# Performance work log

Hardware: AMD Instinct MI355X
Metric: run time of the kernel (lower is better)

The kernel has to match this reference:

```python
import jax, jax.numpy as jnp
import numpy as np

EPS = 1e-5

def layer_norm(x, gamma, beta):
    mu = jnp.mean(x, axis=-1, keepdims=True)
    var = jnp.mean(jnp.square(x - mu), axis=-1, keepdims=True)
    return (x - mu) * jax.lax.rsqrt(var + EPS) * gamma + beta

def setup_inputs() -> dict:
    key = jax.random.key(0)
    ks = jax.random.split(key, 16)
    B, Cq, Hq, Wq = 8, 256, 32, 32
    Cc, Hc, Wc = 512, 64, 64
    def lin(k, fan_in, fan_out):
        lim = 1.0 / np.sqrt(fan_in)
        k1, k2 = jax.random.split(k)
        W = jax.random.uniform(k1, (fan_in, fan_out), jnp.float32, -lim, lim)
        b = jax.random.uniform(k2, (fan_out,), jnp.float32, -lim, lim)
        return W, b
    Wq_, bq = lin(ks[0], Cq, Cq)
    Wk_, bk = lin(ks[1], Cc, Cq)
    Wv_, bv = lin(ks[2], Cc, Cq)
    Wo_, bo = lin(ks[3], Cq, Cq)
    return {
        "query": jax.random.normal(ks[4], (B, Cq, Hq, Wq), jnp.float32),
        "context": jax.random.normal(ks[5], (B, Cc, Hc, Wc), jnp.float32),
        "Wq": Wq_, "bq": bq, "Wk": Wk_, "bk": bk, "Wv": Wv_, "bv": bv,
        "Wo": Wo_, "bo": bo,
        "gq": jnp.ones((Cq,), jnp.float32), "betq": jnp.zeros((Cq,), jnp.float32),
        "gc": jnp.ones((Cc,), jnp.float32), "betc": jnp.zeros((Cc,), jnp.float32),
    }

def reference(query, context, Wq, bq, Wk, bk, Wv, bv, Wo, bo, gq, betq, gc, betc):
    B, Cq, Hq, Wq_sp = query.shape
    _, Cc, Hc, Wc = context.shape
    num_heads = 8
    head_dim = Cq // num_heads
    scale = jnp.sqrt(jnp.float32(head_dim))
    N = Hq * Wq_sp
    # adaptive_avg_pool2d with divisible sizes == average pooling over equal bins
    ctx = context.reshape(B, Cc, Hq, Hc // Hq, Wq_sp, Wc // Wq_sp).mean(axis=(3, 5))
    q_flat = query.reshape(B, Cq, N).transpose(0, 2, 1)          # (B,N,Cq)
    c_flat = ctx.reshape(B, Cc, N).transpose(0, 2, 1)            # (B,N,Cc)
    qn = layer_norm(q_flat, gq, betq)
    cn = layer_norm(c_flat, gc, betc)
    q = (qn @ Wq + bq).reshape(B, N, num_heads, head_dim).transpose(0, 2, 1, 3)
    k = (cn @ Wk + bk).reshape(B, N, num_heads, head_dim).transpose(0, 2, 1, 3)
    v = (cn @ Wv + bv).reshape(B, N, num_heads, head_dim).transpose(0, 2, 1, 3)
    attn = jnp.einsum('bhnd,bhmd->bhnm', q, k) / scale
    attn = jax.nn.softmax(attn, axis=-1)
    out = jnp.einsum('bhnm,bhmd->bhnd', attn, v)
    out = out.transpose(0, 2, 1, 3).reshape(B, N, Cq)
    out = out @ Wo + bo
    out = q_flat + out                                           # residual
    return out.transpose(0, 2, 1).reshape(B, Cq, Hq, Wq_sp)
```

## Files before the change

### kernel.cpp

```cpp
#include <hip/hip_runtime.h>
#include <hip/hip_bf16.h>
#include <cstddef>

#define B_  8
#define CQ  256
#define CC  512
#define N_  1024
#define HQ  32
#define WQ  32
#define NH  8
#define HD  32

typedef __bf16 bf16x8 __attribute__((ext_vector_type(8)));
typedef float f32x4 __attribute__((ext_vector_type(4)));
typedef float f32x16 __attribute__((ext_vector_type(16)));
typedef unsigned int uint4v __attribute__((ext_vector_type(4)));
typedef unsigned short ushort8 __attribute__((ext_vector_type(8)));
typedef unsigned short ushort4v __attribute__((ext_vector_type(4)));

__device__ __forceinline__ unsigned short f2bf(float x) {
    return __builtin_bit_cast(unsigned short, __float2bfloat16(x));
}
__device__ __forceinline__ float bf2f(unsigned short x) {
    return __bfloat162float(__builtin_bit_cast(__hip_bfloat16, x));
}
__device__ __forceinline__ bf16x8 ldb8(const unsigned short* p) {
    return __builtin_bit_cast(bf16x8, *(const ushort8*)p);
}

__global__ __launch_bounds__(256) void prep_k(
    const float* __restrict__ query, const float* __restrict__ context,
    const float* __restrict__ Wq, const float* __restrict__ Wk,
    const float* __restrict__ Wv, const float* __restrict__ Wo,
    const float* __restrict__ gq, const float* __restrict__ betq,
    const float* __restrict__ gc, const float* __restrict__ betc,
    __hip_bfloat16* __restrict__ Wqt, __hip_bfloat16* __restrict__ Wkt,
    __hip_bfloat16* __restrict__ Wvt, __hip_bfloat16* __restrict__ Wot,
    __hip_bfloat16* __restrict__ qn, __hip_bfloat16* __restrict__ cn) {
    __shared__ float T[32][33];
    __shared__ float SsA[32][16];
    __shared__ float S2A[32][16];
    __shared__ float SsB[16][64];
    __shared__ float S2B[16][64];
    __shared__ float Mu[64], Rs[64];

    const int bid = blockIdx.x;
    const int tid = threadIdx.x;

    if (bid < 512) {
        const int x = bid & 15, y = (bid >> 4) & 7, z = bid >> 7;
        const float* W; __hip_bfloat16* Wt; int K;
        switch (z) {
            case 0: W = Wq; Wt = Wqt; K = CQ; break;
            case 1: W = Wk; Wt = Wkt; K = CC; break;
            case 2: W = Wv; Wt = Wvt; K = CC; break;
            default: W = Wo; Wt = Wot; K = CQ; break;
        }
        const int k0 = x * 32;
        if (k0 >= K) return;
        const int c0 = y * 32;
        const int tx = tid & 31, ty = tid >> 5;
        #pragma unroll
        for (int i = 0; i < 4; ++i) {
            const int r = ty + 8 * i;
            T[r][tx] = W[(size_t)(k0 + r) * CQ + c0 + tx];
        }
        __syncthreads();
        #pragma unroll
        for (int i = 0; i < 4; ++i) {
            const int r = ty + 8 * i;
            Wt[(size_t)(c0 + r) * K + k0 + tx] = __float2bfloat16(T[tx][r]);
        }
    } else if (bid < 1024) {
        const int u    = bid - 512;
        const int wqc2 = u & 1, hq = (u >> 1) & 31, b = u >> 6;
        const int pp   = tid & 7;
        const int cg   = tid >> 3;
        const int ch0  = cg * 16;

        const float* Cb = context + ((size_t)b * CC + ch0) * 4096
                        + (size_t)(2 * hq) * 64 + (32 * wqc2 + 4 * pp);
        float pv0[16], pv1[16];
        float ss0 = 0.f, ss1 = 0.f, s20 = 0.f, s21 = 0.f;
        #pragma unroll
        for (int i = 0; i < 16; ++i) {
            const float4 r0 = *(const float4*)(Cb + (size_t)i * 4096);
            const float4 r1 = *(const float4*)(Cb + (size_t)i * 4096 + 64);
            const float v0 = (r0.x + r0.y + r1.x + r1.y) * 0.25f;
            const float v1 = (r0.z + r0.w + r1.z + r1.w) * 0.25f;
            pv0[i] = v0; pv1[i] = v1;
            ss0 += v0; s20 += v0 * v0;
            ss1 += v1; s21 += v1 * v1;
        }
        SsA[cg][2 * pp]     = ss0; S2A[cg][2 * pp]     = s20;
        SsA[cg][2 * pp + 1] = ss1; S2A[cg][2 * pp + 1] = s21;
        __syncthreads();
        if (tid < 16) {
            float ts = 0.f, t2 = 0.f;
            #pragma unroll
            for (int i = 0; i < 32; ++i) { ts += SsA[i][tid]; t2 += S2A[i][tid]; }
            const float mu  = ts * (1.f / CC);
            const float var = t2 * (1.f / CC) - mu * mu;
            Mu[tid] = mu; Rs[tid] = rsqrtf(var + 1e-5f);
        }
        __syncthreads();
        const float mu0 = Mu[2 * pp],     rs0 = Rs[2 * pp];
        const float mu1 = Mu[2 * pp + 1], rs1 = Rs[2 * pp + 1];
        const int pos0 = hq * 32 + wqc2 * 16 + 2 * pp;
        unsigned short* dst = (unsigned short*)cn
            + ((size_t)b * N_ + pos0) * CC + ch0;
        ushort8 a0, a1, b0, b1;
        #pragma unroll
        for (int i = 0; i < 8; ++i) {
            a0[i] = f2bf((pv0[i] - mu0) * rs0 * gc[ch0 + i] + betc[ch0 + i]);
            b0[i] = f2bf((pv1[i] - mu1) * rs1 * gc[ch0 + i] + betc[ch0 + i]);
        }
        #pragma unroll
        for (int i = 0; i < 8; ++i) {
            a1[i] = f2bf((pv0[8 + i] - mu0) * rs0 * gc[ch0 + 8 + i] + betc[ch0 + 8 + i]);
            b1[i] = f2bf((pv1[8 + i] - mu1) * rs1 * gc[ch0 + 8 + i] + betc[ch0 + 8 + i]);
        }
        *(ushort8*)(dst)          = a0;
        *(ushort8*)(dst + 8)      = a1;
        *(ushort8*)(dst + CC)     = b0;
        *(ushort8*)(dst + CC + 8) = b1;
    } else {
        const int u  = bid - 1024;
        const int nt = u & 15, b = u >> 4;
        const int nq = tid & 15;
        const int cg = tid >> 4;
        const int ch0 = cg * 16;
        const int nb  = nt * 64 + 4 * nq;

        const float* Qb = query + ((size_t)b * CQ + ch0) * N_ + nb;
        float qv[64];
        float ps[4] = {0.f, 0.f, 0.f, 0.f};
        float p2[4] = {0.f, 0.f, 0.f, 0.f};
        #pragma unroll
        for (int i = 0; i < 16; ++i) {
            const float4 v = *(const float4*)(Qb + (size_t)i * N_);
            qv[4 * i + 0] = v.x; qv[4 * i + 1] = v.y;
            qv[4 * i + 2] = v.z; qv[4 * i + 3] = v.w;
            ps[0] += v.x; p2[0] += v.x * v.x;
            ps[1] += v.y; p2[1] += v.y * v.y;
            ps[2] += v.z; p2[2] += v.z * v.z;
            ps[3] += v.w; p2[3] += v.w * v.w;
        }
        #pragma unroll
        for (int j = 0; j < 4; ++j) {
            SsB[cg][4 * nq + j] = ps[j];
            S2B[cg][4 * nq + j] = p2[j];
        }
        __syncthreads();
        if (tid < 64) {
            float ts = 0.f, t2 = 0.f;
            #pragma unroll
            for (int i = 0; i < 16; ++i) { ts += SsB[i][tid]; t2 += S2B[i][tid]; }
            const float mu  = ts * (1.f / CQ);
            const float var = t2 * (1.f / CQ) - mu * mu;
            Mu[tid] = mu; Rs[tid] = rsqrtf(var + 1e-5f);
        }
        __syncthreads();
        #pragma unroll
        for (int j = 0; j < 4; ++j) {
            const float mu = Mu[4 * nq + j], rs = Rs[4 * nq + j];
            ushort8 o0, o1;
            #pragma unroll
            for (int i = 0; i < 8; ++i)
                o0[i] = f2bf((qv[4 * i + j] - mu) * rs * gq[ch0 + i] + betq[ch0 + i]);
            #pragma unroll
            for (int i = 0; i < 8; ++i)
                o1[i] = f2bf((qv[4 * (8 + i) + j] - mu) * rs * gq[ch0 + 8 + i] + betq[ch0 + 8 + i]);
            unsigned short* dst = (unsigned short*)qn
                + ((size_t)b * N_ + nb + j) * CQ + ch0;
            *(ushort8*)(dst)     = o0;
            *(ushort8*)(dst + 8) = o1;
        }
    }
}

__global__ __launch_bounds__(256) void proj_all_k(
    const __hip_bfloat16* __restrict__ qn, const __hip_bfloat16* __restrict__ cn,
    const __hip_bfloat16* __restrict__ Wqt, const __hip_bfloat16* __restrict__ Wkt,
    const __hip_bfloat16* __restrict__ Wvt,
    const float* __restrict__ bq, const float* __restrict__ bk,
    const float* __restrict__ bv,
    __hip_bfloat16* __restrict__ Qb, __hip_bfloat16* __restrict__ Kb,
    __hip_bfloat16* __restrict__ Vt, float qsc) {
    __shared__ unsigned short As[64][40];
    __shared__ unsigned short B1[64][40];
    __shared__ unsigned short B2[64][40];

    const int zz = blockIdx.z;
    const int n0 = blockIdx.x * 64;
    const int c0 = blockIdx.y * 64;
    const int tid = threadIdx.x;
    const int wid = tid >> 6, lane = tid & 63;
    const int lg = lane >> 4, ln = lane & 15;
    const int wn0 = (wid & 1) * 32, wc0 = (wid >> 1) * 32;
    const int sr = tid >> 2;
    const int sk = (tid & 3) * 8;

    if (zz >= 8) {
        const int b = zz - 8;
        const unsigned short* Ab = (const unsigned short*)qn + ((size_t)b * N_ + n0) * CQ;
        const unsigned short* Wb = (const unsigned short*)Wqt + (size_t)c0 * CQ;
        f32x4 acc[2][2] = {};
        ushort8 ra = *(const ushort8*)(Ab + (size_t)sr * CQ + sk);
        ushort8 rw = *(const ushort8*)(Wb + (size_t)sr * CQ + sk);
        for (int t = 0; t < 8; ++t) {
            *(ushort8*)&As[sr][sk] = ra;
            *(ushort8*)&B1[sr][sk] = rw;
            __syncthreads();
            if (t < 7) {
                ra = *(const ushort8*)(Ab + (size_t)sr * CQ + (t + 1) * 32 + sk);
                rw = *(const ushort8*)(Wb + (size_t)sr * CQ + (t + 1) * 32 + sk);
            }
            bf16x8 a[2], w[2];
            #pragma unroll
            for (int i = 0; i < 2; ++i) a[i] = ldb8(&As[wn0 + 16 * i + ln][8 * lg]);
            #pragma unroll
            for (int j = 0; j < 2; ++j) w[j] = ldb8(&B1[wc0 + 16 * j + ln][8 * lg]);
            #pragma unroll
            for (int i = 0; i < 2; ++i)
                #pragma unroll
                for (int j = 0; j < 2; ++j)
                    acc[i][j] = __builtin_amdgcn_mfma_f32_16x16x32_bf16(a[i], w[j], acc[i][j], 0, 0, 0);
            __syncthreads();
        }
        #pragma unroll
        for (int j = 0; j < 2; ++j) {
            const int co = c0 + wc0 + 16 * j + ln;
            const int h = co >> 5, d = co & 31;
            const float bb = bq[co];
            #pragma unroll
            for (int i = 0; i < 2; ++i)
                #pragma unroll
                for (int r = 0; r < 4; ++r) {
                    const int n = n0 + wn0 + 16 * i + 4 * lg + r;
                    Qb[(((size_t)b * NH + h) * N_ + n) * HD + d] =
                        __float2bfloat16((acc[i][j][r] + bb) * qsc);
                }
        }
    } else {
        const int b = zz;
        const unsigned short* Ab  = (const unsigned short*)cn + ((size_t)b * N_ + n0) * CC;
        const unsigned short* Wkb = (const unsigned short*)Wkt + (size_t)c0 * CC;
        const unsigned short* Wvb = (const unsigned short*)Wvt + (size_t)c0 * CC;
        f32x4 accK[2][2] = {};
        f32x4 accV[2][2] = {};
        ushort8 ra = *(const ushort8*)(Ab  + (size_t)sr * CC + sk);
        ushort8 rk = *(const ushort8*)(Wkb + (size_t)sr * CC + sk);
        ushort8 rv = *(const ushort8*)(Wvb + (size_t)sr * CC + sk);
        for (int t = 0; t < 16; ++t) {
            *(ushort8*)&As[sr][sk] = ra;
            *(ushort8*)&B1[sr][sk] = rk;
            *(ushort8*)&B2[sr][sk] = rv;
            __syncthreads();
            if (t < 15) {
                ra = *(const ushort8*)(Ab  + (size_t)sr * CC + (t + 1) * 32 + sk);
                rk = *(const ushort8*)(Wkb + (size_t)sr * CC + (t + 1) * 32 + sk);
                rv = *(const ushort8*)(Wvb + (size_t)sr * CC + (t + 1) * 32 + sk);
            }
            bf16x8 a[2], wk[2], wv[2];
            #pragma unroll
            for (int i = 0; i < 2; ++i) {
                a[i]  = ldb8(&As[wn0 + 16 * i + ln][8 * lg]);
                wk[i] = ldb8(&B1[wc0 + 16 * i + ln][8 * lg]);
                wv[i] = ldb8(&B2[wc0 + 16 * i + ln][8 * lg]);
            }
            #pragma unroll
            for (int i = 0; i < 2; ++i)
                #pragma unroll
                for (int j = 0; j < 2; ++j) {
                    accK[i][j] = __builtin_amdgcn_mfma_f32_16x16x32_bf16(a[i], wk[j], accK[i][j], 0, 0, 0);
                    accV[i][j] = __builtin_amdgcn_mfma_f32_16x16x32_bf16(a[i], wv[j], accV[i][j], 0, 0, 0);
                }
            __syncthreads();
        }
        #pragma unroll
        for (int j = 0; j < 2; ++j) {
            const int co = c0 + wc0 + 16 * j + ln;
            const int h = co >> 5, d = co & 31;
            const float bbk = bk[co], bbv = bv[co];
            #pragma unroll
            for (int i = 0; i < 2; ++i) {
                const int nb = n0 + wn0 + 16 * i + 4 * lg;
                #pragma unroll
                for (int r = 0; r < 4; ++r)
                    Kb[(((size_t)b * NH + h) * N_ + nb + r) * HD + d] =
                        __float2bfloat16(accK[i][j][r] + bbk);
                ushort4v o;
                #pragma unroll
                for (int r = 0; r < 4; ++r) o[r] = f2bf(accV[i][j][r] + bbv);
                const int g  = (nb >> 2) & 3;
                const int gp = ((g & 1) << 1) | (g >> 1);
                const int nbp = (nb & ~15) | (gp << 2);
                *(ushort4v*)((unsigned short*)Vt + (((size_t)b * NH + h) * HD + d) * N_ + nbp) = o;
            }
        }
    }
}

__global__ __launch_bounds__(256) void attn32_k(
    const __hip_bfloat16* __restrict__ Q,
    const __hip_bfloat16* __restrict__ K,
    const __hip_bfloat16* __restrict__ Vt,
    __hip_bfloat16* __restrict__ O) {
    __shared__ float accS[2][64][20];
    __shared__ float lwS[2][64];

    const int lin = blockIdx.x + 16 * blockIdx.y;
    const int eff = (lin & 7) * 128 + (lin >> 3);
    const int qt  = eff & 15;
    const int bh  = eff >> 4;
    const int b   = bh >> 3;
    const int h   = bh & 7;
    const int wid  = threadIdx.x >> 6;
    const int lane = threadIdx.x & 63;
    const int l31  = lane & 31;
    const int hh   = lane >> 5;
    const int qsub = wid >> 1;
    const int kvh  = wid & 1;
    const int q0   = qt * 64 + qsub * 32;

    const unsigned short* Qp = (const unsigned short*)Q + ((size_t)bh * N_ + q0) * HD;
    const unsigned short* Kbb = (const unsigned short*)K + (size_t)bh * N_ * HD;
    const unsigned short* Vb = (const unsigned short*)Vt + ((size_t)bh * HD + l31) * N_;

    bf16x8 qB[2];
    #pragma unroll
    for (int m = 0; m < 2; ++m)
        qB[m] = ldb8(Qp + (size_t)l31 * HD + 16 * m + 8 * hh);

    const f32x16 Z = {0.f,0.f,0.f,0.f,0.f,0.f,0.f,0.f,
                      0.f,0.f,0.f,0.f,0.f,0.f,0.f,0.f};
    f32x16 acc = Z;
    float ls0 = 0.f, ls1 = 0.f, ls2 = 0.f, ls3 = 0.f;

    const int kvbase = kvh * 512;
    const unsigned short* kp = Kbb + (size_t)(kvbase + l31) * HD + 8 * hh;
    const unsigned short* vp = Vb + kvbase + 8 * hh;

    bf16x8 kaA[2][4];
    #pragma unroll
    for (int j = 0; j < 4; ++j)
        kaA[0][j] = ldb8(kp + (j >> 1) * 1024 + (j & 1) * 16);

    #pragma unroll
    for (int st = 0; st < 8; ++st) {
        const int cur = st & 1;
        bf16x8 va[4];
        #pragma unroll
        for (int j = 0; j < 4; ++j)
            va[j] = ldb8(vp + st * 64 + 16 * j);
        if (st < 7) {
            const unsigned short* kp2 = kp + (size_t)(st + 1) * 2048;
            #pragma unroll
            for (int j = 0; j < 4; ++j)
                kaA[cur ^ 1][j] = ldb8(kp2 + (j >> 1) * 1024 + (j & 1) * 16);
        }

        f32x16 s0, s1;
        s0 = __builtin_amdgcn_mfma_f32_32x32x16_bf16(kaA[cur][0], qB[0], Z, 0, 0, 0);
        s0 = __builtin_amdgcn_mfma_f32_32x32x16_bf16(kaA[cur][1], qB[1], s0, 0, 0, 0);
        s1 = __builtin_amdgcn_mfma_f32_32x32x16_bf16(kaA[cur][2], qB[0], Z, 0, 0, 0);
        s1 = __builtin_amdgcn_mfma_f32_32x32x16_bf16(kaA[cur][3], qB[1], s1, 0, 0, 0);

        unsigned int pk[2][4][2];
        #pragma unroll
        for (int T = 0; T < 2; ++T) {
            float p[16];
            #pragma unroll
            for (int r = 0; r < 16; ++r)
                p[r] = __builtin_amdgcn_exp2f(T == 0 ? s0[r] : s1[r]);
            #pragma unroll
            for (int r = 0; r < 16; r += 4) {
                ls0 += p[r]; ls1 += p[r + 1]; ls2 += p[r + 2]; ls3 += p[r + 3];
            }
            #pragma unroll
            for (int c = 0; c < 4; ++c) {
                asm("v_cvt_pk_bf16_f32 %0, %1, %2"
                    : "=v"(pk[T][c][0]) : "v"(p[4 * c]), "v"(p[4 * c + 1]));
                asm("v_cvt_pk_bf16_f32 %0, %1, %2"
                    : "=v"(pk[T][c][1]) : "v"(p[4 * c + 2]), "v"(p[4 * c + 3]));
            }
        }

        #pragma unroll
        for (int w = 0; w < 4; ++w) {
            const int T = w >> 1, cp = w & 1;
            uint4v fu = {pk[T][2 * cp][0], pk[T][2 * cp][1],
                         pk[T][2 * cp + 1][0], pk[T][2 * cp + 1][1]};
            const bf16x8 pa = __builtin_bit_cast(bf16x8, fu);
            acc = __builtin_amdgcn_mfma_f32_32x32x16_bf16(pa, va[w], acc, 0, 0, 0);
        }
    }

    const float lsum = (ls0 + ls1) + (ls2 + ls3);
    const float lw = lsum + __shfl_xor(lsum, 32);

    if (kvh == 1) {
        #pragma unroll
        for (int r4 = 0; r4 < 4; ++r4) {
            float4 v = {acc[4 * r4], acc[4 * r4 + 1], acc[4 * r4 + 2], acc[4 * r4 + 3]};
            *(float4*)&accS[qsub][lane][4 * r4] = v;
        }
        lwS[qsub][lane] = lw;
    }
    __syncthreads();
    if (kvh == 0) {
        const float linv = 1.0f / (lw + lwS[qsub][lane]);
        #pragma unroll
        for (int r = 0; r < 16; ++r) {
            const int ql = (r & 3) + 8 * (r >> 2) + 4 * hh;
            const float vv = (acc[r] + accS[qsub][lane][r]) * __shfl(linv, ql);
            O[((size_t)b * N_ + q0 + ql) * CQ + h * HD + l31] = __float2bfloat16(vv);
        }
    }
}

__global__ __launch_bounds__(256) void out_proj_k(const __hip_bfloat16* __restrict__ Ob,
                              const __hip_bfloat16* __restrict__ Wot,
                              const float* __restrict__ bo,
                              const float* __restrict__ query,
                              float* __restrict__ out) {
    __shared__ unsigned short As[64][40];
    __shared__ unsigned short Bs[64][40];
    const int b  = blockIdx.z;
    const int n0 = blockIdx.x * 64;
    const int c0 = blockIdx.y * 64;
    const int tid = threadIdx.x;
    const int wid = tid >> 6, lane = tid & 63;
    const int lg = lane >> 4, ln = lane & 15;
    const int wn0 = (wid & 1) * 32, wc0 = (wid >> 1) * 32;

    const unsigned short* Ab = (const unsigned short*)Ob + ((size_t)b * N_ + n0) * CQ;
    const unsigned short* Wb = (const unsigned short*)Wot + (size_t)c0 * CQ;
    const int sr = tid >> 2;
    const int sk = (tid & 3) * 8;

    f32x4 acc[2][2] = {};
    ushort8 ra = *(const ushort8*)(Ab + (size_t)sr * CQ + sk);
    ushort8 rw = *(const ushort8*)(Wb + (size_t)sr * CQ + sk);

    for (int t = 0; t < 8; ++t) {
        *(ushort8*)&As[sr][sk] = ra;
        *(ushort8*)&Bs[sr][sk] = rw;
        __syncthreads();
        if (t < 7) {
            ra = *(const ushort8*)(Ab + (size_t)sr * CQ + (t + 1) * 32 + sk);
            rw = *(const ushort8*)(Wb + (size_t)sr * CQ + (t + 1) * 32 + sk);
        }
        bf16x8 a[2], w[2];
        #pragma unroll
        for (int i = 0; i < 2; ++i)
            a[i] = ldb8(&As[wn0 + 16 * i + ln][8 * lg]);
        #pragma unroll
        for (int j = 0; j < 2; ++j)
            w[j] = ldb8(&Bs[wc0 + 16 * j + ln][8 * lg]);
        #pragma unroll
        for (int i = 0; i < 2; ++i)
            #pragma unroll
            for (int j = 0; j < 2; ++j)
                acc[i][j] = __builtin_amdgcn_mfma_f32_16x16x32_bf16(a[i], w[j], acc[i][j], 0, 0, 0);
        __syncthreads();
    }

    #pragma unroll
    for (int j = 0; j < 2; ++j) {
        const int co = c0 + wc0 + 16 * j + ln;
        const float bb = bo[co];
        #pragma unroll
        for (int i = 0; i < 2; ++i) {
            const int nb = n0 + wn0 + 16 * i + 4 * lg;
            const float4 res = *(const float4*)&query[((size_t)b * CQ + co) * N_ + nb];
            float4 o;
            o.x = acc[i][j][0] + bb + res.x;
            o.y = acc[i][j][1] + bb + res.y;
            o.z = acc[i][j][2] + bb + res.z;
            o.w = acc[i][j][3] + bb + res.w;
            *(float4*)&out[((size_t)b * CQ + co) * N_ + nb] = o;
        }
    }
}

extern "C" void kernel_launch(void* const* d_in, const int* in_sizes, int n_in,
                              void* d_out, int out_size, void* d_ws, size_t ws_size,
                              hipStream_t stream) {
    const float* query   = (const float*)d_in[0];
    const float* context = (const float*)d_in[1];
    const float* Wq = (const float*)d_in[2];
    const float* bq = (const float*)d_in[3];
    const float* Wk = (const float*)d_in[4];
    const float* bk = (const float*)d_in[5];
    const float* Wv = (const float*)d_in[6];
    const float* bv = (const float*)d_in[7];
    const float* Wo = (const float*)d_in[8];
    const float* bo = (const float*)d_in[9];
    const float* gq   = (const float*)d_in[10];
    const float* betq = (const float*)d_in[11];
    const float* gc   = (const float*)d_in[12];
    const float* betc = (const float*)d_in[13];
    float* out = (float*)d_out;

    char* w = (char*)d_ws;
    __hip_bfloat16* qn  = (__hip_bfloat16*)w;  w += (size_t)B_ * N_ * CQ * 2;
    __hip_bfloat16* cn  = (__hip_bfloat16*)w;  w += (size_t)B_ * N_ * CC * 2;
    __hip_bfloat16* Qb  = (__hip_bfloat16*)w;  w += (size_t)B_ * NH * N_ * HD * 2;
    __hip_bfloat16* Kb  = (__hip_bfloat16*)w;  w += (size_t)B_ * NH * N_ * HD * 2;
    __hip_bfloat16* Vt  = (__hip_bfloat16*)w;  w += (size_t)B_ * NH * HD * N_ * 2;
    __hip_bfloat16* Ob  = (__hip_bfloat16*)w;  w += (size_t)B_ * N_ * CQ * 2;
    __hip_bfloat16* Wqt = (__hip_bfloat16*)w;  w += (size_t)CQ * CQ * 2;
    __hip_bfloat16* Wkt = (__hip_bfloat16*)w;  w += (size_t)CQ * CC * 2;
    __hip_bfloat16* Wvt = (__hip_bfloat16*)w;  w += (size_t)CQ * CC * 2;
    __hip_bfloat16* Wot = (__hip_bfloat16*)w;  w += (size_t)CQ * CQ * 2;

    prep_k<<<dim3(1152), 256, 0, stream>>>(query, context, Wq, Wk, Wv, Wo,
                                           gq, betq, gc, betc,
                                           Wqt, Wkt, Wvt, Wot, qn, cn);

    const float qsc = 0.17677669529663687f * 1.4426950408889634f;
    proj_all_k<<<dim3(16, 4, 16), 256, 0, stream>>>(qn, cn, Wqt, Wkt, Wvt,
                                                    bq, bk, bv, Qb, Kb, Vt, qsc);

    attn32_k<<<dim3(16, 64), 256, 0, stream>>>(Qb, Kb, Vt, Ob);

    out_proj_k<<<dim3(16, 4, 8), 256, 0, stream>>>(Ob, Wot, bo, query, out);
}
```

Before: 66.68 us.

## Widen projection GEMM tiles to 128 columns and use bf16 residual copy

The Q/K/V and output projection GEMMs now use 64x128 output tiles per block (each wave computes 32x64), halving the grid in the channel dimension and reusing each loaded A tile across twice as many output columns. Separately, prep_k writes a bf16 copy of the raw query, which the output projection reads for the residual instead of the fp32 query, halving residual read bytes. The wider tiles raise register use and cut block count to 512/256, which may lower occupancy. The bf16 residual loses precision in the residual add and adds an extra write in prep.

```diff
diff --git a/kernel.cpp b/kernel.cpp
--- a/kernel.cpp
+++ b/kernel.cpp
@@ -36,7 +36,8 @@
     const float* __restrict__ gc, const float* __restrict__ betc,
     __hip_bfloat16* __restrict__ Wqt, __hip_bfloat16* __restrict__ Wkt,
     __hip_bfloat16* __restrict__ Wvt, __hip_bfloat16* __restrict__ Wot,
-    __hip_bfloat16* __restrict__ qn, __hip_bfloat16* __restrict__ cn) {
+    __hip_bfloat16* __restrict__ qn, __hip_bfloat16* __restrict__ cn,
+    __hip_bfloat16* __restrict__ qraw) {
     __shared__ float T[32][33];
     __shared__ float SsA[32][16];
     __shared__ float S2A[32][16];
@@ -147,6 +148,13 @@
             ps[3] += v.w; p2[3] += v.w * v.w;
         }
         #pragma unroll
+        for (int i = 0; i < 16; ++i) {
+            ushort4v o;
+            o[0] = f2bf(qv[4 * i + 0]); o[1] = f2bf(qv[4 * i + 1]);
+            o[2] = f2bf(qv[4 * i + 2]); o[3] = f2bf(qv[4 * i + 3]);
+            *(ushort4v*)((unsigned short*)qraw + ((size_t)b * CQ + ch0 + i) * N_ + nb) = o;
+        }
+        #pragma unroll
         for (int j = 0; j < 4; ++j) {
             SsB[cg][4 * nq + j] = ps[j];
             S2B[cg][4 * nq + j] = p2[j];
@@ -188,48 +196,54 @@
     __hip_bfloat16* __restrict__ Qb, __hip_bfloat16* __restrict__ Kb,
     __hip_bfloat16* __restrict__ Vt, float qsc) {
     __shared__ unsigned short As[64][40];
-    __shared__ unsigned short B1[64][40];
-    __shared__ unsigned short B2[64][40];
+    __shared__ unsigned short B1[128][40];
+    __shared__ unsigned short B2[128][40];
 
     const int zz = blockIdx.z;
     const int n0 = blockIdx.x * 64;
-    const int c0 = blockIdx.y * 64;
+    const int c0 = blockIdx.y * 128;
     const int tid = threadIdx.x;
     const int wid = tid >> 6, lane = tid & 63;
     const int lg = lane >> 4, ln = lane & 15;
-    const int wn0 = (wid & 1) * 32, wc0 = (wid >> 1) * 32;
+    const int wn0 = (wid & 1) * 32, wc0 = (wid >> 1) * 64;
     const int sr = tid >> 2;
     const int sk = (tid & 3) * 8;
+    const int br = tid >> 1;
+    const int bk0 = (tid & 1) * 16;
 
     if (zz >= 8) {
         const int b = zz - 8;
         const unsigned short* Ab = (const unsigned short*)qn + ((size_t)b * N_ + n0) * CQ;
         const unsigned short* Wb = (const unsigned short*)Wqt + (size_t)c0 * CQ;
-        f32x4 acc[2][2] = {};
-        ushort8 ra = *(const ushort8*)(Ab + (size_t)sr * CQ + sk);
-        ushort8 rw = *(const ushort8*)(Wb + (size_t)sr * CQ + sk);
+        f32x4 acc[2][4] = {};
+        ushort8 ra  = *(const ushort8*)(Ab + (size_t)sr * CQ + sk);
+        ushort8 rw0 = *(const ushort8*)(Wb + (size_t)br * CQ + bk0);
+        ushort8 rw1 = *(const ushort8*)(Wb + (size_t)br * CQ + bk0 + 8);
         for (int t = 0; t < 8; ++t) {
-            *(ushort8*)&As[sr][sk] = ra;
-            *(ushort8*)&B1[sr][sk] = rw;
+            *(ushort8*)&As[sr][sk]      = ra;
+            *(ushort8*)&B1[br][bk0]     = rw0;
+            *(ushort8*)&B1[br][bk0 + 8] = rw1;
             __syncthreads();
             if (t < 7) {
-                ra = *(const ushort8*)(Ab + (size_t)sr * CQ + (t + 1) * 32 + sk);
-                rw = *(const ushort8*)(Wb + (size_t)sr * CQ + (t + 1) * 32 + sk);
+                const int k0 = (t + 1) * 32;
+                ra  = *(const ushort8*)(Ab + (size_t)sr * CQ + k0 + sk);
+                rw0 = *(const ushort8*)(Wb + (size_t)br * CQ + k0 + bk0);
+                rw1 = *(const ushort8*)(Wb + (size_t)br * CQ + k0 + bk0 + 8);
             }
-            bf16x8 a[2], w[2];
+            bf16x8 a[2], w[4];
             #pragma unroll
             for (int i = 0; i < 2; ++i) a[i] = ldb8(&As[wn0 + 16 * i + ln][8 * lg]);
             #pragma unroll
-            for (int j = 0; j < 2; ++j) w[j] = ldb8(&B1[wc0 + 16 * j + ln][8 * lg]);
+            for (int j = 0; j < 4; ++j) w[j] = ldb8(&B1[wc0 + 16 * j + ln][8 * lg]);
             #pragma unroll
             for (int i = 0; i < 2; ++i)
                 #pragma unroll
-                for (int j = 0; j < 2; ++j)
+                for (int j = 0; j < 4; ++j)
                     acc[i][j] = __builtin_amdgcn_mfma_f32_16x16x32_bf16(a[i], w[j], acc[i][j], 0, 0, 0);
             __syncthreads();
         }
         #pragma unroll
-        for (int j = 0; j < 2; ++j) {
+        for (int j = 0; j < 4; ++j) {
             const int co = c0 + wc0 + 16 * j + ln;
             const int h = co >> 5, d = co & 31;
             const float bb = bq[co];
@@ -247,39 +261,47 @@
         const unsigned short* Ab  = (const unsigned short*)cn + ((size_t)b * N_ + n0) * CC;
         const unsigned short* Wkb = (const unsigned short*)Wkt + (size_t)c0 * CC;
         const unsigned short* Wvb = (const unsigned short*)Wvt + (size_t)c0 * CC;
-        f32x4 accK[2][2] = {};
-        f32x4 accV[2][2] = {};
-        ushort8 ra = *(const ushort8*)(Ab  + (size_t)sr * CC + sk);
-        ushort8 rk = *(const ushort8*)(Wkb + (size_t)sr * CC + sk);
-        ushort8 rv = *(const ushort8*)(Wvb + (size_t)sr * CC + sk);
+        f32x4 accK[2][4] = {};
+        f32x4 accV[2][4] = {};
+        ushort8 ra  = *(const ushort8*)(Ab  + (size_t)sr * CC + sk);
+        ushort8 rk0 = *(const ushort8*)(Wkb + (size_t)br * CC + bk0);
+        ushort8 rk1 = *(const ushort8*)(Wkb + (size_t)br * CC + bk0 + 8);
+        ushort8 rv0 = *(const ushort8*)(Wvb + (size_t)br * CC + bk0);
+        ushort8 rv1 = *(const ushort8*)(Wvb + (size_t)br * CC + bk0 + 8);
         for (int t = 0; t < 16; ++t) {
-            *(ushort8*)&As[sr][sk] = ra;
-            *(ushort8*)&B1[sr][sk] = rk;
-            *(ushort8*)&B2[sr][sk] = rv;
+            *(ushort8*)&As[sr][sk]      = ra;
+            *(ushort8*)&B1[br][bk0]     = rk0;
+            *(ushort8*)&B1[br][bk0 + 8] = rk1;
+            *(ushort8*)&B2[br][bk0]     = rv0;
+            *(ushort8*)&B2[br][bk0 + 8] = rv1;
             __syncthreads();
             if (t < 15) {
-                ra = *(const ushort8*)(Ab  + (size_t)sr * CC + (t + 1) * 32 + sk);
-                rk = *(const ushort8*)(Wkb + (size_t)sr * CC + (t + 1) * 32 + sk);
-                rv = *(const ushort8*)(Wvb + (size_t)sr * CC + (t + 1) * 32 + sk);
+                const int k0 = (t + 1) * 32;
+                ra  = *(const ushort8*)(Ab  + (size_t)sr * CC + k0 + sk);
+                rk0 = *(const ushort8*)(Wkb + (size_t)br * CC + k0 + bk0);
+                rk1 = *(const ushort8*)(Wkb + (size_t)br * CC + k0 + bk0 + 8);
+                rv0 = *(const ushort8*)(Wvb + (size_t)br * CC + k0 + bk0);
+                rv1 = *(const ushort8*)(Wvb + (size_t)br * CC + k0 + bk0 + 8);
             }
-            bf16x8 a[2], wk[2], wv[2];
-            #pragma unroll
-            for (int i = 0; i < 2; ++i) {
-                a[i]  = ldb8(&As[wn0 + 16 * i + ln][8 * lg]);
-                wk[i] = ldb8(&B1[wc0 + 16 * i + ln][8 * lg]);
-                wv[i] = ldb8(&B2[wc0 + 16 * i + ln][8 * lg]);
+            bf16x8 a[2], wk[4], wv[4];
+            #pragma unroll
+            for (int i = 0; i < 2; ++i) a[i] = ldb8(&As[wn0 + 16 * i + ln][8 * lg]);
+            #pragma unroll
+            for (int j = 0; j < 4; ++j) {
+                wk[j] = ldb8(&B1[wc0 + 16 * j + ln][8 * lg]);
+                wv[j] = ldb8(&B2[wc0 + 16 * j + ln][8 * lg]);
             }
             #pragma unroll
             for (int i = 0; i < 2; ++i)
                 #pragma unroll
-                for (int j = 0; j < 2; ++j) {
+                for (int j = 0; j < 4; ++j) {
                     accK[i][j] = __builtin_amdgcn_mfma_f32_16x16x32_bf16(a[i], wk[j], accK[i][j], 0, 0, 0);
                     accV[i][j] = __builtin_amdgcn_mfma_f32_16x16x32_bf16(a[i], wv[j], accV[i][j], 0, 0, 0);
                 }
             __syncthreads();
         }
         #pragma unroll
-        for (int j = 0; j < 2; ++j) {
+        for (int j = 0; j < 4; ++j) {
             const int co = c0 + wc0 + 16 * j + ln;
             const int h = co >> 5, d = co & 31;
             const float bbk = bk[co], bbv = bv[co];
@@ -423,63 +445,70 @@
 __global__ __launch_bounds__(256) void out_proj_k(const __hip_bfloat16* __restrict__ Ob,
                               const __hip_bfloat16* __restrict__ Wot,
                               const float* __restrict__ bo,
-                              const float* __restrict__ query,
+                              const __hip_bfloat16* __restrict__ qraw,
                               float* __restrict__ out) {
     __shared__ unsigned short As[64][40];
-    __shared__ unsigned short Bs[64][40];
+    __shared__ unsigned short B1[128][40];
     const int b  = blockIdx.z;
     const int n0 = blockIdx.x * 64;
-    const int c0 = blockIdx.y * 64;
+    const int c0 = blockIdx.y * 128;
     const int tid = threadIdx.x;
     const int wid = tid >> 6, lane = tid & 63;
     const int lg = lane >> 4, ln = lane & 15;
-    const int wn0 = (wid & 1) * 32, wc0 = (wid >> 1) * 32;
+    const int wn0 = (wid & 1) * 32, wc0 = (wid >> 1) * 64;
+    const int sr = tid >> 2;
+    const int sk = (tid & 3) * 8;
+    const int br = tid >> 1;
+    const int bk0 = (tid & 1) * 16;
 
     const unsigned short* Ab = (const unsigned short*)Ob + ((size_t)b * N_ + n0) * CQ;
     const unsigned short* Wb = (const unsigned short*)Wot + (size_t)c0 * CQ;
-    const int sr = tid >> 2;
-    const int sk = (tid & 3) * 8;
-
-    f32x4 acc[2][2] = {};
-    ushort8 ra = *(const ushort8*)(Ab + (size_t)sr * CQ + sk);
-    ushort8 rw = *(const ushort8*)(Wb + (size_t)sr * CQ + sk);
+
+    f32x4 acc[2][4] = {};
+    ushort8 ra  = *(const ushort8*)(Ab + (size_t)sr * CQ + sk);
+    ushort8 rw0 = *(const ushort8*)(Wb + (size_t)br * CQ + bk0);
+    ushort8 rw1 = *(const ushort8*)(Wb + (size_t)br * CQ + bk0 + 8);
 
     for (int t = 0; t < 8; ++t) {
-        *(ushort8*)&As[sr][sk] = ra;
-        *(ushort8*)&Bs[sr][sk] = rw;
+        *(ushort8*)&As[sr][sk]      = ra;
+        *(ushort8*)&B1[br][bk0]     = rw0;
+        *(ushort8*)&B1[br][bk0 + 8] = rw1;
         __syncthreads();
         if (t < 7) {
-            ra = *(const ushort8*)(Ab + (size_t)sr * CQ + (t + 1) * 32 + sk);
-            rw = *(const ushort8*)(Wb + (size_t)sr * CQ + (t + 1) * 32 + sk);
-        }
-        bf16x8 a[2], w[2];
+            const int k0 = (t + 1) * 32;
+            ra  = *(const ushort8*)(Ab + (size_t)sr * CQ + k0 + sk);
+            rw0 = *(const ushort8*)(Wb + (size_t)br * CQ + k0 + bk0);
+            rw1 = *(const ushort8*)(Wb + (size_t)br * CQ + k0 + bk0 + 8);
+        }
+        bf16x8 a[2], w[4];
         #pragma unroll
         for (int i = 0; i < 2; ++i)
             a[i] = ldb8(&As[wn0 + 16 * i + ln][8 * lg]);
         #pragma unroll
-        for (int j = 0; j < 2; ++j)
-            w[j] = ldb8(&Bs[wc0 + 16 * j + ln][8 * lg]);
+        for (int j = 0; j < 4; ++j)
+            w[j] = ldb8(&B1[wc0 + 16 * j + ln][8 * lg]);
         #pragma unroll
         for (int i = 0; i < 2; ++i)
             #pragma unroll
-            for (int j = 0; j < 2; ++j)
+            for (int j = 0; j < 4; ++j)
                 acc[i][j] = __builtin_amdgcn_mfma_f32_16x16x32_bf16(a[i], w[j], acc[i][j], 0, 0, 0);
         __syncthreads();
     }
 
     #pragma unroll
-    for (int j = 0; j < 2; ++j) {
+    for (int j = 0; j < 4; ++j) {
         const int co = c0 + wc0 + 16 * j + ln;
         const float bb = bo[co];
         #pragma unroll
         for (int i = 0; i < 2; ++i) {
             const int nb = n0 + wn0 + 16 * i + 4 * lg;
-            const float4 res = *(const float4*)&query[((size_t)b * CQ + co) * N_ + nb];
+            const ushort4v res = *(const ushort4v*)((const unsigned short*)qraw
+                + ((size_t)b * CQ + co) * N_ + nb);
             float4 o;
-            o.x = acc[i][j][0] + bb + res.x;
-            o.y = acc[i][j][1] + bb + res.y;
-            o.z = acc[i][j][2] + bb + res.z;
-            o.w = acc[i][j][3] + bb + res.w;
+            o.x = acc[i][j][0] + bb + bf2f(res[0]);
+            o.y = acc[i][j][1] + bb + bf2f(res[1]);
+            o.z = acc[i][j][2] + bb + bf2f(res[2]);
+            o.w = acc[i][j][3] + bb + bf2f(res[3]);
             *(float4*)&out[((size_t)b * CQ + co) * N_ + nb] = o;
         }
     }
@@ -505,26 +534,27 @@
     float* out = (float*)d_out;
 
     char* w = (char*)d_ws;
-    __hip_bfloat16* qn  = (__hip_bfloat16*)w;  w += (size_t)B_ * N_ * CQ * 2;
-    __hip_bfloat16* cn  = (__hip_bfloat16*)w;  w += (size_t)B_ * N_ * CC * 2;
-    __hip_bfloat16* Qb  = (__hip_bfloat16*)w;  w += (size_t)B_ * NH * N_ * HD * 2;
-    __hip_bfloat16* Kb  = (__hip_bfloat16*)w;  w += (size_t)B_ * NH * N_ * HD * 2;
-    __hip_bfloat16* Vt  = (__hip_bfloat16*)w;  w += (size_t)B_ * NH * HD * N_ * 2;
-    __hip_bfloat16* Ob  = (__hip_bfloat16*)w;  w += (size_t)B_ * N_ * CQ * 2;
-    __hip_bfloat16* Wqt = (__hip_bfloat16*)w;  w += (size_t)CQ * CQ * 2;
-    __hip_bfloat16* Wkt = (__hip_bfloat16*)w;  w += (size_t)CQ * CC * 2;
-    __hip_bfloat16* Wvt = (__hip_bfloat16*)w;  w += (size_t)CQ * CC * 2;
-    __hip_bfloat16* Wot = (__hip_bfloat16*)w;  w += (size_t)CQ * CQ * 2;
+    __hip_bfloat16* qn   = (__hip_bfloat16*)w;  w += (size_t)B_ * N_ * CQ * 2;
+    __hip_bfloat16* cn   = (__hip_bfloat16*)w;  w += (size_t)B_ * N_ * CC * 2;
+    __hip_bfloat16* qraw = (__hip_bfloat16*)w;  w += (size_t)B_ * CQ * N_ * 2;
+    __hip_bfloat16* Qb   = (__hip_bfloat16*)w;  w += (size_t)B_ * NH * N_ * HD * 2;
+    __hip_bfloat16* Kb   = (__hip_bfloat16*)w;  w += (size_t)B_ * NH * N_ * HD * 2;
+    __hip_bfloat16* Vt   = (__hip_bfloat16*)w;  w += (size_t)B_ * NH * HD * N_ * 2;
+    __hip_bfloat16* Ob   = (__hip_bfloat16*)w;  w += (size_t)B_ * N_ * CQ * 2;
+    __hip_bfloat16* Wqt  = (__hip_bfloat16*)w;  w += (size_t)CQ * CQ * 2;
+    __hip_bfloat16* Wkt  = (__hip_bfloat16*)w;  w += (size_t)CQ * CC * 2;
+    __hip_bfloat16* Wvt  = (__hip_bfloat16*)w;  w += (size_t)CQ * CC * 2;
+    __hip_bfloat16* Wot  = (__hip_bfloat16*)w;  w += (size_t)CQ * CQ * 2;
 
     prep_k<<<dim3(1152), 256, 0, stream>>>(query, context, Wq, Wk, Wv, Wo,
                                            gq, betq, gc, betc,
-                                           Wqt, Wkt, Wvt, Wot, qn, cn);
+                                           Wqt, Wkt, Wvt, Wot, qn, cn, qraw);
 
     const float qsc = 0.17677669529663687f * 1.4426950408889634f;
-    proj_all_k<<<dim3(16, 4, 16), 256, 0, stream>>>(qn, cn, Wqt, Wkt, Wvt,
+    proj_all_k<<<dim3(16, 2, 16), 256, 0, stream>>>(qn, cn, Wqt, Wkt, Wvt,
                                                     bq, bk, bv, Qb, Kb, Vt, qsc);
 
     attn32_k<<<dim3(16, 64), 256, 0, stream>>>(Qb, Kb, Vt, Ob);
 
-    out_proj_k<<<dim3(16, 4, 8), 256, 0, stream>>>(Ob, Wot, bo, query, out);
-}
+    out_proj_k<<<dim3(16, 2, 8), 256, 0, stream>>>(Ob, Wot, bo, qraw, out);
+}
```

After: 68.36 us. 2.5% more time.
